# Optimization experiments

Measured on AMD Instinct MI355X. Metric: run time of the kernel, lower is better.

The kernel has to match this reference:

```python
import jax, jax.numpy as jnp
import numpy as np

B, L, D, F = 1024, 2, 1024, 32768


def setup_inputs() -> dict:
    key = jax.random.key(0)
    k1, k2, k3 = jax.random.split(key, 3)
    scale = 1.0 / np.sqrt(D)
    x = jax.random.normal(k1, (B, L, D), dtype=jnp.float32)
    W_enc = jax.random.normal(k2, (L, D, F), dtype=jnp.float32) * scale
    b_enc = jnp.zeros((F,), dtype=jnp.float32)
    W_dec = jax.random.normal(k3, (L, F, D), dtype=jnp.float32) * scale
    b_dec = jnp.zeros((L, D), dtype=jnp.float32)
    return {"x": x, "W_enc": W_enc, "b_enc": b_enc, "W_dec": W_dec, "b_dec": b_dec}


def reference(x, W_enc, b_enc, W_dec, b_dec):
    # Encoder: per-layer projection summed over layers, then ReLU (CrossCoderEncoder.forward)
    # f_per_layer: einsum('bld,ldf->blf'); sum over l fused into the contraction.
    f = jax.nn.relu(jnp.einsum('bld,ldf->bf', x, W_enc) + b_enc)  # [B, F]
    # Decoder (linear branch == math of the embedding_bag sparse branch):
    # x_hat = einsum('bf,lfd->bld') + bias
    x_hat = jnp.einsum('bf,lfd->bld', f, W_dec) + b_dec  # [B, L, D]
    return x_hat
```

## Files before the change

kernel.cpp:

```cpp
#include <hip/hip_runtime.h>
#include <hip/hip_bf16.h>

#define B_  1024
#define L_  2
#define D_  1024
#define F_  32768
#define K1  (L_*D_)
#define M_  B_
#define N2  (L_*D_)
#define SPLITK 4
#define KC  (F_/SPLITK)

#define BM 128
#define BN 128
#define BK 32
#define LDK 40

typedef __attribute__((ext_vector_type(4))) float  f32x4;
typedef __attribute__((ext_vector_type(8))) __bf16 bf16x8;
typedef __attribute__((ext_vector_type(4))) __bf16 bf16x4;

__global__ __launch_bounds__(256, 2) void gemm1_enc(
    const float* __restrict__ X, const float* __restrict__ We,
    const float* __restrict__ be, __bf16* __restrict__ Fout)
{
    __shared__ __bf16 As[BM][LDK];
    __shared__ __bf16 Bs[BN][LDK];

    const int tid = threadIdx.x;
    const int m0 = blockIdx.x * BM;
    const int n0 = blockIdx.y * BN;

    const int lane = tid & 63;
    const int w  = tid >> 6;
    const int wr = w >> 1, wc = w & 1;
    const int g  = lane >> 4;
    const int r  = lane & 15;

    const int a_row = tid >> 3;
    const int a_c4  = tid & 7;
    const int b_kb  = tid >> 5;
    const int b_nb  = tid & 31;

    f32x4 acc[4][4] = {};

    f32x4 aP[4];
    f32x4 bP[4];

    const float* Aptr = X + (size_t)m0 * K1;
    const float* Bptr = We + n0;

    auto loadA = [&](int k0) {
        #pragma unroll
        for (int p = 0; p < 4; ++p) {
            int row = a_row + 32*p;
            aP[p] = *(const f32x4*)(Aptr + (size_t)row*K1 + k0 + a_c4*4);
        }
    };
    auto loadB = [&](int k0) {
        #pragma unroll
        for (int i = 0; i < 4; ++i) {
            bP[i] = *(const f32x4*)(Bptr + (size_t)(k0 + b_kb*4 + i)*F_ + b_nb*4);
        }
    };
    auto stageA = [&]() {
        #pragma unroll
        for (int p = 0; p < 4; ++p) {
            int row = a_row + 32*p;
            bf16x4 v;
            v[0] = (__bf16)aP[p][0]; v[1] = (__bf16)aP[p][1];
            v[2] = (__bf16)aP[p][2]; v[3] = (__bf16)aP[p][3];
            *(bf16x4*)&As[row][a_c4*4] = v;
        }
    };
    auto stageB = [&]() {
        #pragma unroll
        for (int j = 0; j < 4; ++j) {
            bf16x4 v;
            v[0] = (__bf16)bP[0][j]; v[1] = (__bf16)bP[1][j];
            v[2] = (__bf16)bP[2][j]; v[3] = (__bf16)bP[3][j];
            *(bf16x4*)&Bs[b_nb*4 + j][b_kb*4] = v;
        }
    };

    loadA(0); loadB(0);
    for (int k0 = 0; k0 < K1; k0 += BK) {
        stageA(); stageB();
        __syncthreads();
        if (k0 + BK < K1) { loadA(k0 + BK); loadB(k0 + BK); }

        bf16x8 a[4], b[4];
        #pragma unroll
        for (int i = 0; i < 4; ++i)
            a[i] = *(const bf16x8*)&As[wr*64 + i*16 + r][g*8];
        #pragma unroll
        for (int j = 0; j < 4; ++j)
            b[j] = *(const bf16x8*)&Bs[wc*64 + j*16 + r][g*8];
        #pragma unroll
        for (int i = 0; i < 4; ++i)
            #pragma unroll
            for (int j = 0; j < 4; ++j)
                acc[i][j] = __builtin_amdgcn_mfma_f32_16x16x32_bf16(
                    a[i], b[j], acc[i][j], 0, 0, 0);
        __syncthreads();
    }

    #pragma unroll
    for (int j = 0; j < 4; ++j) {
        int col = n0 + wc*64 + j*16 + r;
        float bv = be[col];
        #pragma unroll
        for (int i = 0; i < 4; ++i) {
            #pragma unroll
            for (int v = 0; v < 4; ++v) {
                int row = m0 + wr*64 + i*16 + g*4 + v;
                float z = acc[i][j][v] + bv;
                z = z > 0.f ? z : 0.f;
                Fout[(size_t)row * F_ + col] = (__bf16)z;
            }
        }
    }
}

__global__ __launch_bounds__(256, 2) void gemm2_dec(
    const __bf16* __restrict__ Fin, const float* __restrict__ Wd,
    float* __restrict__ Cp)
{
    __shared__ __bf16 As[BM][LDK];
    __shared__ __bf16 Bs[BN][LDK];

    const int tid = threadIdx.x;
    const int m0 = blockIdx.x * BM;
    const int n0 = blockIdx.y * BN;
    const int s  = blockIdx.z;
    const int kbase = s * KC;

    const int lane = tid & 63;
    const int w  = tid >> 6;
    const int wr = w >> 1, wc = w & 1;
    const int g  = lane >> 4;
    const int r  = lane & 15;

    const int a_row = tid >> 2;
    const int a_c8  = tid & 3;
    const int b_kb  = tid >> 5;
    const int b_nb  = tid & 31;

    f32x4 acc[4][4] = {};

    f32x4 aP[2];
    f32x4 bP[4];

    const int ldec = n0 >> 10;
    const float* Bptr = Wd + (size_t)ldec * F_ * D_ + (n0 & (D_-1));
    const __bf16* Aptr = Fin + (size_t)m0 * F_ + kbase;

    auto loadA = [&](int k0) {
        #pragma unroll
        for (int p = 0; p < 2; ++p) {
            int row = a_row + 64*p;
            aP[p] = *(const f32x4*)(Aptr + (size_t)row*F_ + k0 + a_c8*8);
        }
    };
    auto loadB = [&](int k0) {
        #pragma unroll
        for (int i = 0; i < 4; ++i) {
            bP[i] = *(const f32x4*)(Bptr + (size_t)(kbase + k0 + b_kb*4 + i)*D_ + b_nb*4);
        }
    };
    auto stageA = [&]() {
        #pragma unroll
        for (int p = 0; p < 2; ++p) {
            int row = a_row + 64*p;
            *(f32x4*)&As[row][a_c8*8] = aP[p];
        }
    };
    auto stageB = [&]() {
        #pragma unroll
        for (int j = 0; j < 4; ++j) {
            bf16x4 v;
            v[0] = (__bf16)bP[0][j]; v[1] = (__bf16)bP[1][j];
            v[2] = (__bf16)bP[2][j]; v[3] = (__bf16)bP[3][j];
            *(bf16x4*)&Bs[b_nb*4 + j][b_kb*4] = v;
        }
    };

    loadA(0); loadB(0);
    for (int k0 = 0; k0 < KC; k0 += BK) {
        stageA(); stageB();
        __syncthreads();
        if (k0 + BK < KC) { loadA(k0 + BK); loadB(k0 + BK); }

        bf16x8 a[4], b[4];
        #pragma unroll
        for (int i = 0; i < 4; ++i)
            a[i] = *(const bf16x8*)&As[wr*64 + i*16 + r][g*8];
        #pragma unroll
        for (int j = 0; j < 4; ++j)
            b[j] = *(const bf16x8*)&Bs[wc*64 + j*16 + r][g*8];
        #pragma unroll
        for (int i = 0; i < 4; ++i)
            #pragma unroll
            for (int j = 0; j < 4; ++j)
                acc[i][j] = __builtin_amdgcn_mfma_f32_16x16x32_bf16(
                    a[i], b[j], acc[i][j], 0, 0, 0);
        __syncthreads();
    }

    #pragma unroll
    for (int j = 0; j < 4; ++j) {
        int col = n0 + wc*64 + j*16 + r;
        #pragma unroll
        for (int i = 0; i < 4; ++i) {
            #pragma unroll
            for (int v = 0; v < 4; ++v) {
                int row = m0 + wr*64 + i*16 + g*4 + v;
                Cp[((size_t)s*M_ + row)*N2 + col] = acc[i][j][v];
            }
        }
    }
}

__global__ __launch_bounds__(256) void reduce_add(
    const float* __restrict__ Cp, const float* __restrict__ bd,
    float* __restrict__ out)
{
    const size_t idx = ((size_t)blockIdx.x * 256 + threadIdx.x) * 4;
    f32x4 acc = {};
    #pragma unroll
    for (int s = 0; s < SPLITK; ++s) {
        f32x4 c = *(const f32x4*)(Cp + (size_t)s * M_ * N2 + idx);
        acc += c;
    }
    f32x4 b = *(const f32x4*)(bd + (idx & (N2 - 1)));
    *(f32x4*)(out + idx) = acc + b;
}

extern "C" void kernel_launch(void* const* d_in, const int* in_sizes, int n_in,
                              void* d_out, int out_size, void* d_ws, size_t ws_size,
                              hipStream_t stream) {
    const float* x  = (const float*)d_in[0];
    const float* We = (const float*)d_in[1];
    const float* be = (const float*)d_in[2];
    const float* Wd = (const float*)d_in[3];
    const float* bd = (const float*)d_in[4];
    float* out = (float*)d_out;

    __bf16* f  = (__bf16*)d_ws;
    float*  Cp = (float*)((char*)d_ws + (size_t)M_ * F_ * sizeof(__bf16));

    gemm1_enc<<<dim3(M_/BM, F_/BN), 256, 0, stream>>>(x, We, be, f);
    gemm2_dec<<<dim3(M_/BM, N2/BN, SPLITK), 256, 0, stream>>>(f, Wd, Cp);
    reduce_add<<<dim3((M_*(size_t)N2)/(4*256)), 256, 0, stream>>>(Cp, bd, out);
}
```

Before: 1.001 ms.

## Remap blocks per XCD, restage LDS layouts, use direct global-to-LDS loads for decoder A

Both GEMMs switch to a 1D grid whose block index is decoded so that blocks landing on the same XCD share N tiles and walk all M tiles, which is meant to improve L2 reuse of weight columns. The staging of A and B into shared memory changes: the weight tile is now read as one scalar column per thread over 16 k values and written as two 8-wide bf16 vectors into padded rows of 72 elements. Fragment offsets are precomputed. The decoder's bf16 activation tile is copied straight into LDS with global_load_lds, skipping the register round trip, though it is no longer prefetched one step ahead and relies on the barrier for ordering. The scalar strided weight loads may coalesce worse than the previous float4 loads.

```diff
diff --git a/kernel.cpp b/kernel.cpp
--- a/kernel.cpp
+++ b/kernel.cpp
@@ -14,74 +14,85 @@
 #define BM 128
 #define BN 128
 #define BK 32
-#define LDK 40
+#define ROWE 72
 
 typedef __attribute__((ext_vector_type(4))) float  f32x4;
 typedef __attribute__((ext_vector_type(8))) __bf16 bf16x8;
-typedef __attribute__((ext_vector_type(4))) __bf16 bf16x4;
+
+__device__ inline void glds16(const void* g, void* l) {
+    __builtin_amdgcn_global_load_lds(
+        (const __attribute__((address_space(1))) unsigned int*)g,
+        (__attribute__((address_space(3))) unsigned int*)l, 16, 0, 0);
+}
 
 __global__ __launch_bounds__(256, 2) void gemm1_enc(
     const float* __restrict__ X, const float* __restrict__ We,
     const float* __restrict__ be, __bf16* __restrict__ Fout)
 {
-    __shared__ __bf16 As[BM][LDK];
-    __shared__ __bf16 Bs[BN][LDK];
+    __shared__ __bf16 As[BM * ROWE];
+    __shared__ __bf16 Bs[BN * ROWE];
+
+    const int bid = blockIdx.x;
+    const int xcd = bid & 7;
+    const int j   = bid >> 3;
+    const int m0  = (j & 7) * BM;
+    const int n0  = (xcd * 32 + (j >> 3)) * BN;
 
     const int tid = threadIdx.x;
-    const int m0 = blockIdx.x * BM;
-    const int n0 = blockIdx.y * BN;
-
     const int lane = tid & 63;
     const int w  = tid >> 6;
     const int wr = w >> 1, wc = w & 1;
     const int g  = lane >> 4;
     const int r  = lane & 15;
 
-    const int a_row = tid >> 3;
-    const int a_c4  = tid & 7;
-    const int b_kb  = tid >> 5;
-    const int b_nb  = tid & 31;
+    const int am = tid >> 1;
+    const int ah = tid & 1;
+    const int bn  = tid & 127;
+    const int bc2 = tid >> 7;
 
     f32x4 acc[4][4] = {};
-
     f32x4 aP[4];
-    f32x4 bP[4];
+    float bP[16];
 
     const float* Aptr = X + (size_t)m0 * K1;
-    const float* Bptr = We + n0;
+    const float* Bptr = We + n0 + bn;
 
     auto loadA = [&](int k0) {
         #pragma unroll
-        for (int p = 0; p < 4; ++p) {
-            int row = a_row + 32*p;
-            aP[p] = *(const f32x4*)(Aptr + (size_t)row*K1 + k0 + a_c4*4);
-        }
+        for (int q = 0; q < 4; ++q)
+            aP[q] = *(const f32x4*)(Aptr + (size_t)am*K1 + k0 + ah*16 + q*4);
     };
     auto loadB = [&](int k0) {
         #pragma unroll
-        for (int i = 0; i < 4; ++i) {
-            bP[i] = *(const f32x4*)(Bptr + (size_t)(k0 + b_kb*4 + i)*F_ + b_nb*4);
-        }
+        for (int kk = 0; kk < 16; ++kk)
+            bP[kk] = Bptr[(size_t)(k0 + bc2*16 + kk) * F_];
     };
     auto stageA = [&]() {
-        #pragma unroll
-        for (int p = 0; p < 4; ++p) {
-            int row = a_row + 32*p;
-            bf16x4 v;
-            v[0] = (__bf16)aP[p][0]; v[1] = (__bf16)aP[p][1];
-            v[2] = (__bf16)aP[p][2]; v[3] = (__bf16)aP[p][3];
-            *(bf16x4*)&As[row][a_c4*4] = v;
-        }
+        bf16x8 v0, v1;
+        #pragma unroll
+        for (int e = 0; e < 4; ++e) {
+            v0[e]   = (__bf16)aP[0][e];  v0[e+4] = (__bf16)aP[1][e];
+            v1[e]   = (__bf16)aP[2][e];  v1[e+4] = (__bf16)aP[3][e];
+        }
+        *(bf16x8*)&As[am*ROWE + (ah*2  )*8] = v0;
+        *(bf16x8*)&As[am*ROWE + (ah*2+1)*8] = v1;
     };
     auto stageB = [&]() {
-        #pragma unroll
-        for (int j = 0; j < 4; ++j) {
-            bf16x4 v;
-            v[0] = (__bf16)bP[0][j]; v[1] = (__bf16)bP[1][j];
-            v[2] = (__bf16)bP[2][j]; v[3] = (__bf16)bP[3][j];
-            *(bf16x4*)&Bs[b_nb*4 + j][b_kb*4] = v;
-        }
-    };
+        bf16x8 v0, v1;
+        #pragma unroll
+        for (int e = 0; e < 8; ++e) {
+            v0[e] = (__bf16)bP[e];
+            v1[e] = (__bf16)bP[8+e];
+        }
+        *(bf16x8*)&Bs[bn*ROWE + (bc2*2  )*8] = v0;
+        *(bf16x8*)&Bs[bn*ROWE + (bc2*2+1)*8] = v1;
+    };
+
+    int aOff[4], bOff[4];
+    #pragma unroll
+    for (int i = 0; i < 4; ++i) aOff[i] = (wr*64 + i*16 + r)*ROWE + g*8;
+    #pragma unroll
+    for (int jj = 0; jj < 4; ++jj) bOff[jj] = (wc*64 + jj*16 + r)*ROWE + g*8;
 
     loadA(0); loadB(0);
     for (int k0 = 0; k0 < K1; k0 += BK) {
@@ -91,30 +102,28 @@
 
         bf16x8 a[4], b[4];
         #pragma unroll
+        for (int i = 0; i < 4; ++i) a[i] = *(const bf16x8*)&As[aOff[i]];
+        #pragma unroll
+        for (int jj = 0; jj < 4; ++jj) b[jj] = *(const bf16x8*)&Bs[bOff[jj]];
+        #pragma unroll
         for (int i = 0; i < 4; ++i)
-            a[i] = *(const bf16x8*)&As[wr*64 + i*16 + r][g*8];
-        #pragma unroll
-        for (int j = 0; j < 4; ++j)
-            b[j] = *(const bf16x8*)&Bs[wc*64 + j*16 + r][g*8];
-        #pragma unroll
-        for (int i = 0; i < 4; ++i)
-            #pragma unroll
-            for (int j = 0; j < 4; ++j)
-                acc[i][j] = __builtin_amdgcn_mfma_f32_16x16x32_bf16(
-                    a[i], b[j], acc[i][j], 0, 0, 0);
-        __syncthreads();
-    }
-
-    #pragma unroll
-    for (int j = 0; j < 4; ++j) {
-        int col = n0 + wc*64 + j*16 + r;
+            #pragma unroll
+            for (int jj = 0; jj < 4; ++jj)
+                acc[i][jj] = __builtin_amdgcn_mfma_f32_16x16x32_bf16(
+                    a[i], b[jj], acc[i][jj], 0, 0, 0);
+        __syncthreads();
+    }
+
+    #pragma unroll
+    for (int jj = 0; jj < 4; ++jj) {
+        int col = n0 + wc*64 + jj*16 + r;
         float bv = be[col];
         #pragma unroll
         for (int i = 0; i < 4; ++i) {
             #pragma unroll
             for (int v = 0; v < 4; ++v) {
                 int row = m0 + wr*64 + i*16 + g*4 + v;
-                float z = acc[i][j][v] + bv;
+                float z = acc[i][jj][v] + bv;
                 z = z > 0.f ? z : 0.f;
                 Fout[(size_t)row * F_ + col] = (__bf16)z;
             }
@@ -126,96 +135,92 @@
     const __bf16* __restrict__ Fin, const float* __restrict__ Wd,
     float* __restrict__ Cp)
 {
-    __shared__ __bf16 As[BM][LDK];
-    __shared__ __bf16 Bs[BN][LDK];
+    __shared__ __bf16 As2[BM * BK];
+    __shared__ __bf16 Bs[BN * ROWE];
+
+    const int bid = blockIdx.x;
+    const int xcd = bid & 7;
+    const int j   = bid >> 3;
+    const int m0  = (j & 7) * BM;
+    const int pair = xcd * 8 + (j >> 3);
+    const int s   = pair & 3;
+    const int n0  = (pair >> 2) * BN;
+    const int kbase = s * KC;
 
     const int tid = threadIdx.x;
-    const int m0 = blockIdx.x * BM;
-    const int n0 = blockIdx.y * BN;
-    const int s  = blockIdx.z;
-    const int kbase = s * KC;
-
     const int lane = tid & 63;
     const int w  = tid >> 6;
     const int wr = w >> 1, wc = w & 1;
     const int g  = lane >> 4;
     const int r  = lane & 15;
 
-    const int a_row = tid >> 2;
-    const int a_c8  = tid & 3;
-    const int b_kb  = tid >> 5;
-    const int b_nb  = tid & 31;
+    const int bn  = tid & 127;
+    const int bc2 = tid >> 7;
 
     f32x4 acc[4][4] = {};
-
-    f32x4 aP[2];
-    f32x4 bP[4];
+    float bP[16];
 
     const int ldec = n0 >> 10;
-    const float* Bptr = Wd + (size_t)ldec * F_ * D_ + (n0 & (D_-1));
+    const float* Bptr = Wd + (size_t)ldec * F_ * D_ + (n0 & (D_-1)) + bn;
     const __bf16* Aptr = Fin + (size_t)m0 * F_ + kbase;
 
-    auto loadA = [&](int k0) {
+    auto loadB = [&](int k0) {
+        #pragma unroll
+        for (int kk = 0; kk < 16; ++kk)
+            bP[kk] = Bptr[(size_t)(kbase + k0 + bc2*16 + kk) * D_];
+    };
+    auto stageB = [&]() {
+        bf16x8 v0, v1;
+        #pragma unroll
+        for (int e = 0; e < 8; ++e) {
+            v0[e] = (__bf16)bP[e];
+            v1[e] = (__bf16)bP[8+e];
+        }
+        *(bf16x8*)&Bs[bn*ROWE + (bc2*2  )*8] = v0;
+        *(bf16x8*)&Bs[bn*ROWE + (bc2*2+1)*8] = v1;
+    };
+
+    int aOff[4], bOff[4];
+    #pragma unroll
+    for (int i = 0; i < 4; ++i) aOff[i] = (wr*64 + i*16 + r)*BK + g*8;
+    #pragma unroll
+    for (int jj = 0; jj < 4; ++jj) bOff[jj] = (wc*64 + jj*16 + r)*ROWE + g*8;
+
+    loadB(0);
+    for (int k0 = 0; k0 < KC; k0 += BK) {
         #pragma unroll
         for (int p = 0; p < 2; ++p) {
-            int row = a_row + 64*p;
-            aP[p] = *(const f32x4*)(Aptr + (size_t)row*F_ + k0 + a_c8*8);
-        }
-    };
-    auto loadB = [&](int k0) {
-        #pragma unroll
-        for (int i = 0; i < 4; ++i) {
-            bP[i] = *(const f32x4*)(Bptr + (size_t)(kbase + k0 + b_kb*4 + i)*D_ + b_nb*4);
-        }
-    };
-    auto stageA = [&]() {
-        #pragma unroll
-        for (int p = 0; p < 2; ++p) {
-            int row = a_row + 64*p;
-            *(f32x4*)&As[row][a_c8*8] = aP[p];
-        }
-    };
-    auto stageB = [&]() {
-        #pragma unroll
-        for (int j = 0; j < 4; ++j) {
-            bf16x4 v;
-            v[0] = (__bf16)bP[0][j]; v[1] = (__bf16)bP[1][j];
-            v[2] = (__bf16)bP[2][j]; v[3] = (__bf16)bP[3][j];
-            *(bf16x4*)&Bs[b_nb*4 + j][b_kb*4] = v;
-        }
-    };
-
-    loadA(0); loadB(0);
-    for (int k0 = 0; k0 < KC; k0 += BK) {
-        stageA(); stageB();
-        __syncthreads();
-        if (k0 + BK < KC) { loadA(k0 + BK); loadB(k0 + BK); }
+            int ch = p*256 + tid;
+            int m = ch >> 2, c = ch & 3;
+            glds16(Aptr + (size_t)m*F_ + k0 + c*8, &As2[ch*8]);
+        }
+        stageB();
+        __syncthreads();
+        if (k0 + BK < KC) loadB(k0 + BK);
 
         bf16x8 a[4], b[4];
         #pragma unroll
+        for (int i = 0; i < 4; ++i) a[i] = *(const bf16x8*)&As2[aOff[i]];
+        #pragma unroll
+        for (int jj = 0; jj < 4; ++jj) b[jj] = *(const bf16x8*)&Bs[bOff[jj]];
+        #pragma unroll
         for (int i = 0; i < 4; ++i)
-            a[i] = *(const bf16x8*)&As[wr*64 + i*16 + r][g*8];
-        #pragma unroll
-        for (int j = 0; j < 4; ++j)
-            b[j] = *(const bf16x8*)&Bs[wc*64 + j*16 + r][g*8];
-        #pragma unroll
-        for (int i = 0; i < 4; ++i)
-            #pragma unroll
-            for (int j = 0; j < 4; ++j)
-                acc[i][j] = __builtin_amdgcn_mfma_f32_16x16x32_bf16(
-                    a[i], b[j], acc[i][j], 0, 0, 0);
-        __syncthreads();
-    }
-
-    #pragma unroll
-    for (int j = 0; j < 4; ++j) {
-        int col = n0 + wc*64 + j*16 + r;
+            #pragma unroll
+            for (int jj = 0; jj < 4; ++jj)
+                acc[i][jj] = __builtin_amdgcn_mfma_f32_16x16x32_bf16(
+                    a[i], b[jj], acc[i][jj], 0, 0, 0);
+        __syncthreads();
+    }
+
+    #pragma unroll
+    for (int jj = 0; jj < 4; ++jj) {
+        int col = n0 + wc*64 + jj*16 + r;
         #pragma unroll
         for (int i = 0; i < 4; ++i) {
             #pragma unroll
             for (int v = 0; v < 4; ++v) {
                 int row = m0 + wr*64 + i*16 + g*4 + v;
-                Cp[((size_t)s*M_ + row)*N2 + col] = acc[i][j][v];
+                Cp[((size_t)s*M_ + row)*N2 + col] = acc[i][jj][v];
             }
         }
     }
@@ -249,7 +254,7 @@
     __bf16* f  = (__bf16*)d_ws;
     float*  Cp = (float*)((char*)d_ws + (size_t)M_ * F_ * sizeof(__bf16));
 
-    gemm1_enc<<<dim3(M_/BM, F_/BN), 256, 0, stream>>>(x, We, be, f);
-    gemm2_dec<<<dim3(M_/BM, N2/BN, SPLITK), 256, 0, stream>>>(f, Wd, Cp);
+    gemm1_enc<<<dim3((M_/BM)*(F_/BN)), 256, 0, stream>>>(x, We, be, f);
+    gemm2_dec<<<dim3((M_/BM)*(N2/BN)*SPLITK), 256, 0, stream>>>(f, Wd, Cp);
     reduce_add<<<dim3((M_*(size_t)N2)/(4*256)), 256, 0, stream>>>(Cp, bd, out);
 }
```

Result: faster. 979.1 us (-2.2%).
